# Kernel optimization log

Measured on AMD Instinct MI355X. Metric: run time of the kernel, lower is better.

Reference implementation:

```python
import jax, jax.numpy as jnp
import numpy as np

B, L, DIM, N_STATE, K_CONV = 2, 2048, 1024, 16, 4


def setup_inputs() -> dict:
    key = jax.random.key(0)
    ks = jax.random.split(key, 6)
    sc = lambda k, shape, s: jax.random.normal(k, shape, jnp.float32) * s
    return {
        "x": jax.random.normal(ks[0], (B, L, DIM), jnp.float32),
        "in_proj_w": sc(ks[1], (2 * DIM, DIM), 0.02),
        "conv_w": sc(ks[2], (DIM, 1, K_CONV), 0.1),
        "conv_b": jnp.zeros((DIM,), jnp.float32),
        "x_proj_w": sc(ks[3], (2 * N_STATE + DIM, DIM), 0.02),
        "D_param": jnp.ones((DIM,), jnp.float32),
        "out_proj_w": sc(ks[4], (DIM, DIM), 0.02),
    }


def reference(x, in_proj_w, conv_w, conv_b, x_proj_w, D_param, out_proj_w):
    b, l, d = x.shape
    n = (x_proj_w.shape[0] - d) // 2
    k = conv_w.shape[-1]
    # A buffer: -[1..n] broadcast over channels -> [d, n]
    A = -(jnp.arange(1, n + 1, dtype=x.dtype)[None, :] * jnp.ones((d, 1), x.dtype))

    xz = x @ in_proj_w.T                       # [b, l, 2d]
    x_c, z = xz[..., :d], xz[..., d:]

    # depthwise causal conv (torch pads both sides k-1 then truncates to l == left-pad k-1)
    xc = jnp.transpose(x_c, (0, 2, 1))          # [b, d, l]
    xc = jax.lax.conv_general_dilated(
        xc, conv_w, window_strides=(1,), padding=[(k - 1, 0)],
        dimension_numbers=("NCH", "OIH", "NCH"), feature_group_count=d)
    xc = xc + conv_b[None, :, None]
    xc = jax.nn.silu(jnp.transpose(xc, (0, 2, 1)))  # [b, l, d]

    x_dbl = xc @ x_proj_w.T                    # [b, l, 2n + d]
    B_ssm = x_dbl[..., :n]                     # [b, l, n]
    C_ssm = x_dbl[..., n:2 * n]                # [b, l, n]
    dt = jax.nn.softplus(x_dbl[..., 2 * n:])   # [b, l, d]

    dA = jnp.exp(dt[..., None] * A[None, None])            # [b, l, d, n]
    dBx = (dt[..., None] * B_ssm[:, :, None, :]) * xc[..., None]  # dB * x, [b, l, d, n]

    def step(h, inputs):
        dA_t, dBx_t, C_t = inputs              # [b,d,n], [b,d,n], [b,n]
        h = h * dA_t + dBx_t
        y_t = jnp.einsum("bdn,bn->bd", h, C_t)
        return h, y_t

    h0 = jnp.zeros((b, d, n), x.dtype)
    _, ys = jax.lax.scan(
        step, h0,
        (jnp.moveaxis(dA, 1, 0), jnp.moveaxis(dBx, 1, 0), jnp.moveaxis(C_ssm, 1, 0)))
    y = jnp.moveaxis(ys, 0, 1) + D_param * xc  # [b, l, d]
    y = y * jax.nn.silu(z)
    return y @ out_proj_w.T
```

## Files before the change

### kernel.cpp

```cpp
#include <hip/hip_runtime.h>
#include <cmath>

#define BB   2
#define LL   2048
#define DIMD 1024
#define NS   16
#define KC   4
#define ML   (BB*LL)
#define XZ_N (2*DIMD)
#define XD_N (2*NS + DIMD)
#define LC   16
#define NC   (LL/LC)

typedef __attribute__((ext_vector_type(8))) short bf16x8;
typedef __attribute__((ext_vector_type(4))) float f32x4;

__device__ __forceinline__ unsigned short f2bf(float f) {
    union { float f; unsigned u; } v; v.f = f;
    unsigned r = v.u + 0x7FFF + ((v.u >> 16) & 1);
    return (unsigned short)(r >> 16);
}
__device__ __forceinline__ float bf2f(unsigned short u) {
    union { unsigned u; float f; } v; v.u = (unsigned)u << 16;
    return v.f;
}
__device__ __forceinline__ float silu_f(float a) {
    return a / (1.f + __expf(-a));
}
__device__ __forceinline__ void dt_decay(float raw, float& dt, float& e) {
    const float t = __expf(fminf(raw, 80.f));
    e  = 1.f / (1.f + t);
    dt = (raw > 15.f) ? raw : -__logf(e);
}

__global__ __launch_bounds__(256) void cvt_all(
    const float* __restrict__ s0, unsigned short* __restrict__ d0, int n0,
    const float* __restrict__ s1, unsigned short* __restrict__ d1, int n1,
    const float* __restrict__ s2, unsigned short* __restrict__ d2, int n2,
    const float* __restrict__ s3, unsigned short* __restrict__ d3, int n3)
{
    int i = blockIdx.x * blockDim.x + threadIdx.x;
    const float* src; unsigned short* dst;
    if (i < n0)                { src = s0; dst = d0; }
    else if ((i -= n0) < n1)   { src = s1; dst = d1; }
    else if ((i -= n1) < n2)   { src = s2; dst = d2; }
    else if ((i -= n2) < n3)   { src = s3; dst = d3; }
    else return;
    float4 f = ((const float4*)src)[i];
    ushort4 o;
    o.x = f2bf(f.x); o.y = f2bf(f.y); o.z = f2bf(f.z); o.w = f2bf(f.w);
    ((ushort4*)dst)[i] = o;
}

__global__ __launch_bounds__(256) void gemm_mfma_bt(
    const unsigned short* __restrict__ A,
    const unsigned short* __restrict__ Bw,
    float* __restrict__ C,
    unsigned short* __restrict__ zb,
    int M, int N, int K, int nsplit)
{
    __shared__ short As[128 * 64];
    __shared__ short Bs[64 * 64];

    const int tid  = threadIdx.x;
    const int lane = tid & 63;
    const int wave = tid >> 6;
    const int bm = blockIdx.y * 128;
    const int bn = blockIdx.x * 64;
    const int wm = wave * 32;
    const int l15  = lane & 15;
    const int quad = lane >> 4;

    f32x4 acc[2][4];
    #pragma unroll
    for (int i = 0; i < 2; ++i)
        #pragma unroll
        for (int j = 0; j < 4; ++j)
            acc[i][j] = (f32x4){0.f, 0.f, 0.f, 0.f};

    for (int k0 = 0; k0 < K; k0 += 64) {
        __syncthreads();
        #pragma unroll
        for (int q = 0; q < 4; ++q) {
            const int ci = q * 256 + tid;
            const int r  = ci >> 3;
            const int cc = (ci & 7) ^ (r & 7);
            short* ldsA = As + (size_t)(q * 256 + (tid & ~63)) * 8;
            const unsigned short* ga = A + (size_t)(bm + r) * K + k0 + cc * 8;
            __builtin_amdgcn_global_load_lds(
                (const __attribute__((address_space(1))) void*)ga,
                (__attribute__((address_space(3))) void*)ldsA, 16, 0, 0);
        }
        #pragma unroll
        for (int q = 0; q < 2; ++q) {
            const int ci = q * 256 + tid;
            const int r  = ci >> 3;
            const int cc = (ci & 7) ^ (r & 7);
            short* ldsB = Bs + (size_t)(q * 256 + (tid & ~63)) * 8;
            int rb = bn + r; if (rb > N - 1) rb = N - 1;
            const unsigned short* gb = Bw + (size_t)rb * K + k0 + cc * 8;
            __builtin_amdgcn_global_load_lds(
                (const __attribute__((address_space(1))) void*)gb,
                (__attribute__((address_space(3))) void*)ldsB, 16, 0, 0);
        }
        __syncthreads();

        #pragma unroll
        for (int kh = 0; kh < 2; ++kh) {
            bf16x8 af[2], bfr[4];
            #pragma unroll
            for (int i = 0; i < 2; ++i) {
                const int row = wm + i * 16 + l15;
                const int pc  = (kh * 4 + quad) ^ (row & 7);
                af[i] = *(const bf16x8*)(As + row * 64 + pc * 8);
            }
            #pragma unroll
            for (int j = 0; j < 4; ++j) {
                const int row = j * 16 + l15;
                const int pc  = (kh * 4 + quad) ^ (row & 7);
                bfr[j] = *(const bf16x8*)(Bs + row * 64 + pc * 8);
            }
            #pragma unroll
            for (int i = 0; i < 2; ++i)
                #pragma unroll
                for (int j = 0; j < 4; ++j)
                    acc[i][j] = __builtin_amdgcn_mfma_f32_16x16x32_bf16(
                        af[i], bfr[j], acc[i][j], 0, 0, 0);
        }
    }

    #pragma unroll
    for (int i = 0; i < 2; ++i) {
        const int rbase = bm + wm + i * 16 + quad * 4;
        #pragma unroll
        for (int j = 0; j < 4; ++j) {
            const int col = bn + j * 16 + l15;
            if (col < nsplit) {
                #pragma unroll
                for (int r = 0; r < 4; ++r)
                    C[(size_t)(rbase + r) * nsplit + col] = acc[i][j][r];
            } else if (col < N) {
                const int zc = col - nsplit;
                #pragma unroll
                for (int r = 0; r < 4; ++r)
                    zb[(size_t)(rbase + r) * DIMD + zc] = f2bf(silu_f(acc[i][j][r]));
            }
        }
    }
}

__global__ __launch_bounds__(256) void conv_silu(const float* __restrict__ xcraw,
                                                 const float* __restrict__ w,
                                                 const float* __restrict__ bias,
                                                 float* __restrict__ xc,
                                                 unsigned short* __restrict__ xcb)
{
    const int i4 = blockIdx.x * blockDim.x + threadIdx.x;
    if (i4 >= ML * DIMD / 4) return;
    const int dq = i4 & (DIMD / 4 - 1);
    const int bl = i4 >> 8;
    const int l  = bl & (LL - 1);

    const float4 wq0 = ((const float4*)w)[dq * 4 + 0];
    const float4 wq1 = ((const float4*)w)[dq * 4 + 1];
    const float4 wq2 = ((const float4*)w)[dq * 4 + 2];
    const float4 wq3 = ((const float4*)w)[dq * 4 + 3];
    const float4 bv  = ((const float4*)bias)[dq];

    const float* p = xcraw + (size_t)bl * DIMD + dq * 4;
    const float4 z4 = make_float4(0.f, 0.f, 0.f, 0.f);
    const float4 x0 = (l >= 3) ? *(const float4*)(p - 3 * DIMD) : z4;
    const float4 x1 = (l >= 2) ? *(const float4*)(p - 2 * DIMD) : z4;
    const float4 x2 = (l >= 1) ? *(const float4*)(p - 1 * DIMD) : z4;
    const float4 x3 = *(const float4*)p;

    float4 a;
    a.x = bv.x + wq0.x*x0.x + wq0.y*x1.x + wq0.z*x2.x + wq0.w*x3.x;
    a.y = bv.y + wq1.x*x0.y + wq1.y*x1.y + wq1.z*x2.y + wq1.w*x3.y;
    a.z = bv.z + wq2.x*x0.z + wq2.y*x1.z + wq2.z*x2.z + wq2.w*x3.z;
    a.w = bv.w + wq3.x*x0.w + wq3.y*x1.w + wq3.z*x2.w + wq3.w*x3.w;

    float4 v;
    v.x = silu_f(a.x); v.y = silu_f(a.y); v.z = silu_f(a.z); v.w = silu_f(a.w);

    ((float4*)xc)[i4] = v;
    ushort4 o;
    o.x = f2bf(v.x); o.y = f2bf(v.y); o.z = f2bf(v.z); o.w = f2bf(v.w);
    ((ushort4*)xcb)[i4] = o;
}

__global__ __launch_bounds__(256) void scan_part1(const float* __restrict__ xdbl,
                                                  const float* __restrict__ xc,
                                                  float* __restrict__ hfin,
                                                  float* __restrict__ Ssum)
{
    __shared__ float Bsh[LC][NS];

    const int tid = threadIdx.x;
    const int idx = blockIdx.x * 256 + tid;
    const int d   = idx & (DIMD - 1);
    const int bc  = idx >> 10;
    const int c   = bc & (NC - 1);
    const int b   = bc >> 7;
    const int l0  = c * LC;

    const float* xdbl_p = xdbl + ((size_t)b * LL + l0) * XD_N;
    const float* xc_p   = xc   + ((size_t)b * LL + l0) * DIMD + d;

    if (tid < LC * NS / 4) {
        const int l = tid >> 2, q = tid & 3;
        ((float4*)&Bsh[l][0])[q] = ((const float4*)(xdbl_p + (size_t)l * XD_N))[q];
    }
    __syncthreads();

    float raw[LC], xcv[LC];
    #pragma unroll
    for (int i = 0; i < LC; ++i) raw[i] = xdbl_p[(size_t)i * XD_N + 2 * NS + d];
    #pragma unroll
    for (int i = 0; i < LC; ++i) xcv[i] = xc_p[(size_t)i * DIMD];

    float e[LC], dx[LC];
    float S = 0.f;
    #pragma unroll
    for (int i = 0; i < LC; ++i) {
        float dt, ev;
        dt_decay(raw[i], dt, ev);
        S += dt;
        e[i]  = ev;
        dx[i] = dt * xcv[i];
    }

    float h[NS];
    #pragma unroll
    for (int n = 0; n < NS; ++n) h[n] = 0.f;

    #pragma unroll
    for (int i = 0; i < LC; ++i) {
        const float4* BC = (const float4*)&Bsh[i][0];
        const float4 B0 = BC[0], B1 = BC[1], B2 = BC[2], B3 = BC[3];
        const float ev = e[i], dxv = dx[i];
        const float e2 = ev * ev, e4 = e2 * e2;
        float p0 = ev, p1 = e2, p2 = e2 * ev, p3 = e4;
        h[0]  = fmaf(h[0],  p0, dxv * B0.x);
        h[1]  = fmaf(h[1],  p1, dxv * B0.y);
        h[2]  = fmaf(h[2],  p2, dxv * B0.z);
        h[3]  = fmaf(h[3],  p3, dxv * B0.w);
        p0 *= e4; p1 *= e4; p2 *= e4; p3 *= e4;
        h[4]  = fmaf(h[4],  p0, dxv * B1.x);
        h[5]  = fmaf(h[5],  p1, dxv * B1.y);
        h[6]  = fmaf(h[6],  p2, dxv * B1.z);
        h[7]  = fmaf(h[7],  p3, dxv * B1.w);
        p0 *= e4; p1 *= e4; p2 *= e4; p3 *= e4;
        h[8]  = fmaf(h[8],  p0, dxv * B2.x);
        h[9]  = fmaf(h[9],  p1, dxv * B2.y);
        h[10] = fmaf(h[10], p2, dxv * B2.z);
        h[11] = fmaf(h[11], p3, dxv * B2.w);
        p0 *= e4; p1 *= e4; p2 *= e4; p3 *= e4;
        h[12] = fmaf(h[12], p0, dxv * B3.x);
        h[13] = fmaf(h[13], p1, dxv * B3.y);
        h[14] = fmaf(h[14], p2, dxv * B3.z);
        h[15] = fmaf(h[15], p3, dxv * B3.w);
    }

    float4* hf = (float4*)(hfin + (size_t)idx * NS);
    #pragma unroll
    for (int n = 0; n < 4; ++n) hf[n] = ((float4*)h)[n];
    Ssum[idx] = S;
}

__global__ __launch_bounds__(256) void scan_combine(float* __restrict__ hfin,
                                                    const float* __restrict__ Ssum)
{
    const int idx = blockIdx.x * blockDim.x + threadIdx.x;
    const int n = idx & (NS - 1);
    const int d = (idx >> 4) & (DIMD - 1);
    const int b = idx >> 14;
    const float np1 = (float)(n + 1);

    float hc = 0.f;
    for (int c0 = 0; c0 < NC; c0 += 8) {
        float Sb[8], hb[8], eb[8];
        #pragma unroll
        for (int j = 0; j < 8; ++j) {
            const size_t base = ((size_t)(b * NC + c0 + j) * DIMD + d);
            Sb[j] = Ssum[base];
            hb[j] = hfin[base * NS + n];
        }
        #pragma unroll
        for (int j = 0; j < 8; ++j) eb[j] = __expf(-Sb[j] * np1);
        #pragma unroll
        for (int j = 0; j < 8; ++j) {
            const size_t o = ((size_t)(b * NC + c0 + j) * DIMD + d) * NS + n;
            hfin[o] = hc;
            hc = fmaf(hc, eb[j], hb[j]);
        }
    }
}

__global__ __launch_bounds__(256) void scan_part2(const float* __restrict__ xdbl,
                                                  const float* __restrict__ xc,
                                                  const unsigned short* __restrict__ zb,
                                                  const float* __restrict__ hfin,
                                                  const float* __restrict__ Dp,
                                                  unsigned short* __restrict__ yout)
{
    __shared__ float BCs[LC][2 * NS];

    const int tid = threadIdx.x;
    const int idx = blockIdx.x * 256 + tid;
    const int d   = idx & (DIMD - 1);
    const int bc  = idx >> 10;
    const int c   = bc & (NC - 1);
    const int b   = bc >> 7;
    const int l0  = c * LC;

    const float* xdbl_p = xdbl + ((size_t)b * LL + l0) * XD_N;
    const float* xc_p   = xc   + ((size_t)b * LL + l0) * DIMD + d;
    const unsigned short* zb_p = zb + ((size_t)b * LL + l0) * DIMD + d;
    unsigned short* y_p = yout + ((size_t)b * LL + l0) * DIMD + d;

    if (tid < LC * 2 * NS / 4) {
        const int l = tid >> 3, q = tid & 7;
        ((float4*)&BCs[l][0])[q] = ((const float4*)(xdbl_p + (size_t)l * XD_N))[q];
    }
    __syncthreads();

    float raw[LC], xcv[LC], zg[LC];
    #pragma unroll
    for (int i = 0; i < LC; ++i) raw[i] = xdbl_p[(size_t)i * XD_N + 2 * NS + d];
    #pragma unroll
    for (int i = 0; i < LC; ++i) xcv[i] = xc_p[(size_t)i * DIMD];
    #pragma unroll
    for (int i = 0; i < LC; ++i) zg[i] = bf2f(zb_p[(size_t)i * DIMD]);

    float e[LC], dx[LC];
    #pragma unroll
    for (int i = 0; i < LC; ++i) {
        float dt, ev;
        dt_decay(raw[i], dt, ev);
        e[i]  = ev;
        dx[i] = dt * xcv[i];
    }

    const float Dv = Dp[d];
    float h[NS];
    {
        const float4* hf = (const float4*)(hfin + (size_t)idx * NS);
        #pragma unroll
        for (int n = 0; n < 4; ++n) ((float4*)h)[n] = hf[n];
    }

    #pragma unroll
    for (int i = 0; i < LC; ++i) {
        const float4* BC = (const float4*)&BCs[i][0];
        const float4 B0 = BC[0], B1 = BC[1], B2 = BC[2], B3 = BC[3];
        const float4 C0 = BC[4], C1 = BC[5], C2 = BC[6], C3 = BC[7];
        const float ev = e[i], dxv = dx[i];
        const float e2 = ev * ev, e4 = e2 * e2;
        float p0 = ev, p1 = e2, p2 = e2 * ev, p3 = e4;
        float y0, y1, y2, y3;
        h[0]  = fmaf(h[0],  p0, dxv * B0.x); y0 = h[0]  * C0.x;
        h[1]  = fmaf(h[1],  p1, dxv * B0.y); y1 = h[1]  * C0.y;
        h[2]  = fmaf(h[2],  p2, dxv * B0.z); y2 = h[2]  * C0.z;
        h[3]  = fmaf(h[3],  p3, dxv * B0.w); y3 = h[3]  * C0.w;
        p0 *= e4; p1 *= e4; p2 *= e4; p3 *= e4;
        h[4]  = fmaf(h[4],  p0, dxv * B1.x); y0 = fmaf(h[4],  C1.x, y0);
        h[5]  = fmaf(h[5],  p1, dxv * B1.y); y1 = fmaf(h[5],  C1.y, y1);
        h[6]  = fmaf(h[6],  p2, dxv * B1.z); y2 = fmaf(h[6],  C1.z, y2);
        h[7]  = fmaf(h[7],  p3, dxv * B1.w); y3 = fmaf(h[7],  C1.w, y3);
        p0 *= e4; p1 *= e4; p2 *= e4; p3 *= e4;
        h[8]  = fmaf(h[8],  p0, dxv * B2.x); y0 = fmaf(h[8],  C2.x, y0);
        h[9]  = fmaf(h[9],  p1, dxv * B2.y); y1 = fmaf(h[9],  C2.y, y1);
        h[10] = fmaf(h[10], p2, dxv * B2.z); y2 = fmaf(h[10], C2.z, y2);
        h[11] = fmaf(h[11], p3, dxv * B2.w); y3 = fmaf(h[11], C2.w, y3);
        p0 *= e4; p1 *= e4; p2 *= e4; p3 *= e4;
        h[12] = fmaf(h[12], p0, dxv * B3.x); y0 = fmaf(h[12], C3.x, y0);
        h[13] = fmaf(h[13], p1, dxv * B3.y); y1 = fmaf(h[13], C3.y, y1);
        h[14] = fmaf(h[14], p2, dxv * B3.z); y2 = fmaf(h[14], C3.z, y2);
        h[15] = fmaf(h[15], p3, dxv * B3.w); y3 = fmaf(h[15], C3.w, y3);

        const float y  = (y0 + y1) + (y2 + y3);
        const float yv = fmaf(Dv, xcv[i], y);
        y_p[(size_t)i * DIMD] = f2bf(yv * zg[i]);
    }
}

extern "C" void kernel_launch(void* const* d_in, const int* in_sizes, int n_in,
                              void* d_out, int out_size, void* d_ws, size_t ws_size,
                              hipStream_t stream)
{
    const float* x          = (const float*)d_in[0];
    const float* in_proj_w  = (const float*)d_in[1];
    const float* conv_w     = (const float*)d_in[2];
    const float* conv_b     = (const float*)d_in[3];
    const float* x_proj_w   = (const float*)d_in[4];
    const float* D_param    = (const float*)d_in[5];
    const float* out_proj_w = (const float*)d_in[6];
    float* out = (float*)d_out;

    float* xcraw = (float*)d_ws;
    float* xc    = xcraw + (size_t)ML * DIMD;
    float* xdbl  = xc    + (size_t)ML * DIMD;
    unsigned short* zb  = (unsigned short*)(xdbl + (size_t)ML * XD_N);
    unsigned short* xb  = zb  + (size_t)ML * DIMD;
    unsigned short* xcb = xb  + (size_t)ML * DIMD;
    unsigned short* wb1 = xcb + (size_t)ML * DIMD;
    unsigned short* wb2 = wb1 + (size_t)XZ_N * DIMD;
    unsigned short* wb3 = wb2 + (size_t)XD_N * DIMD;
    float* hfin = (float*)(wb3 + (size_t)DIMD * DIMD);
    float* Ssum = hfin + (size_t)BB * NC * DIMD * NS;
    unsigned short* yb  = xb;

    const int n0 = ML * DIMD / 4, n1 = XZ_N * DIMD / 4,
              n2 = XD_N * DIMD / 4, n3 = DIMD * DIMD / 4;
    const int ncvt = n0 + n1 + n2 + n3;

    cvt_all<<<(ncvt + 255) / 256, 256, 0, stream>>>(
        x, xb, n0, in_proj_w, wb1, n1, x_proj_w, wb2, n2, out_proj_w, wb3, n3);

    gemm_mfma_bt<<<dim3(XZ_N / 64, ML / 128), 256, 0, stream>>>(
        xb, wb1, xcraw, zb, ML, XZ_N, DIMD, DIMD);

    conv_silu<<<(ML * DIMD / 4) / 256, 256, 0, stream>>>(
        xcraw, conv_w, conv_b, xc, xcb);

    gemm_mfma_bt<<<dim3((XD_N + 63) / 64, ML / 128), 256, 0, stream>>>(
        xcb, wb2, xdbl, nullptr, ML, XD_N, DIMD, XD_N);

    scan_part1<<<(BB * NC * DIMD) / 256, 256, 0, stream>>>(xdbl, xc, hfin, Ssum);
    scan_combine<<<(BB * DIMD * NS) / 256, 256, 0, stream>>>(hfin, Ssum);
    scan_part2<<<(BB * NC * DIMD) / 256, 256, 0, stream>>>(xdbl, xc, zb, hfin,
                                                           D_param, yb);

    gemm_mfma_bt<<<dim3(DIMD / 64, ML / 128), 256, 0, stream>>>(
        yb, wb3, out, nullptr, ML, DIMD, DIMD, DIMD);
}
```

Baseline: 213.3 us.

## Double-buffer LDS tiles in bf16 GEMM and remap workgroups across XCDs

The GEMM kernel now keeps two LDS buffers for the A and B tiles. It issues the global-to-LDS loads for the next K slice before running the MFMAs on the current one, so load latency overlaps with compute. This replaces the two barriers per iteration with a single waitcnt plus barrier. It also permutes workgroup IDs in chunks of eight so that neighbouring output tiles land on the same XCD, which should improve L2 reuse. In exchange, LDS use doubles, which may lower occupancy, and the remap assumes the grid size is divisible by eight.

```diff
diff --git a/kernel.cpp b/kernel.cpp
--- a/kernel.cpp
+++ b/kernel.cpp
@@ -59,14 +59,21 @@
     unsigned short* __restrict__ zb,
     int M, int N, int K, int nsplit)
 {
-    __shared__ short As[128 * 64];
-    __shared__ short Bs[64 * 64];
+    __shared__ short As[2][128 * 64];
+    __shared__ short Bs[2][64 * 64];
+
+    const int nwg  = gridDim.x * gridDim.y;
+    int wgid = blockIdx.y * gridDim.x + blockIdx.x;
+    const int cpx = nwg >> 3;
+    wgid = (wgid & 7) * cpx + (wgid >> 3);
+    const int bx = wgid % gridDim.x;
+    const int by = wgid / gridDim.x;
 
     const int tid  = threadIdx.x;
     const int lane = tid & 63;
     const int wave = tid >> 6;
-    const int bm = blockIdx.y * 128;
-    const int bn = blockIdx.x * 64;
+    const int bm = by * 128;
+    const int bn = bx * 64;
     const int wm = wave * 32;
     const int l15  = lane & 15;
     const int quad = lane >> 4;
@@ -78,14 +85,15 @@
         for (int j = 0; j < 4; ++j)
             acc[i][j] = (f32x4){0.f, 0.f, 0.f, 0.f};
 
-    for (int k0 = 0; k0 < K; k0 += 64) {
-        __syncthreads();
+    const int NK = K >> 6;
+
+    auto stage = [&](int s, int k0) {
         #pragma unroll
         for (int q = 0; q < 4; ++q) {
             const int ci = q * 256 + tid;
             const int r  = ci >> 3;
             const int cc = (ci & 7) ^ (r & 7);
-            short* ldsA = As + (size_t)(q * 256 + (tid & ~63)) * 8;
+            short* ldsA = &As[s][0] + (size_t)(q * 256 + (tid & ~63)) * 8;
             const unsigned short* ga = A + (size_t)(bm + r) * K + k0 + cc * 8;
             __builtin_amdgcn_global_load_lds(
                 (const __attribute__((address_space(1))) void*)ga,
@@ -96,15 +104,25 @@
             const int ci = q * 256 + tid;
             const int r  = ci >> 3;
             const int cc = (ci & 7) ^ (r & 7);
-            short* ldsB = Bs + (size_t)(q * 256 + (tid & ~63)) * 8;
+            short* ldsB = &Bs[s][0] + (size_t)(q * 256 + (tid & ~63)) * 8;
             int rb = bn + r; if (rb > N - 1) rb = N - 1;
             const unsigned short* gb = Bw + (size_t)rb * K + k0 + cc * 8;
             __builtin_amdgcn_global_load_lds(
                 (const __attribute__((address_space(1))) void*)gb,
                 (__attribute__((address_space(3))) void*)ldsB, 16, 0, 0);
         }
-        __syncthreads();
-
+    };
+
+    stage(0, 0);
+    asm volatile("s_waitcnt vmcnt(0)" ::: "memory");
+    __builtin_amdgcn_s_barrier();
+
+    int cur = 0;
+    for (int t = 0; t < NK; ++t) {
+        if (t + 1 < NK) stage(cur ^ 1, (t + 1) * 64);
+
+        const short* Ab = &As[cur][0];
+        const short* Bb = &Bs[cur][0];
         #pragma unroll
         for (int kh = 0; kh < 2; ++kh) {
             bf16x8 af[2], bfr[4];
@@ -112,13 +130,13 @@
             for (int i = 0; i < 2; ++i) {
                 const int row = wm + i * 16 + l15;
                 const int pc  = (kh * 4 + quad) ^ (row & 7);
-                af[i] = *(const bf16x8*)(As + row * 64 + pc * 8);
+                af[i] = *(const bf16x8*)(Ab + row * 64 + pc * 8);
             }
             #pragma unroll
             for (int j = 0; j < 4; ++j) {
                 const int row = j * 16 + l15;
                 const int pc  = (kh * 4 + quad) ^ (row & 7);
-                bfr[j] = *(const bf16x8*)(Bs + row * 64 + pc * 8);
+                bfr[j] = *(const bf16x8*)(Bb + row * 64 + pc * 8);
             }
             #pragma unroll
             for (int i = 0; i < 2; ++i)
@@ -127,6 +145,12 @@
                     acc[i][j] = __builtin_amdgcn_mfma_f32_16x16x32_bf16(
                         af[i], bfr[j], acc[i][j], 0, 0, 0);
         }
+
+        if (t + 1 < NK) {
+            asm volatile("s_waitcnt vmcnt(0)" ::: "memory");
+            __builtin_amdgcn_s_barrier();
+        }
+        cur ^= 1;
     }
 
     #pragma unroll
```

Result: no change. 214.5 us (+0.6%).
